# Kernel tuning notes

Hardware: AMD Instinct MI355X
Metric: run time of the kernel (lower is better)

Reference implementation:

```python
import jax, jax.numpy as jnp
import numpy as np

B, S, D = 4, 4096, 2048


def setup_inputs() -> dict:
    key = jax.random.key(0)
    ks = jax.random.split(key, 9)
    std = 1.0 / np.sqrt(D)
    inp = {
        "x": jax.random.normal(ks[0], (B, S, D), dtype=jnp.float32),
        "Wq": jax.random.normal(ks[1], (D, D), dtype=jnp.float32) * std,
        "bq": jnp.zeros((D,), dtype=jnp.float32),
        "Wk": jax.random.normal(ks[2], (D, D), dtype=jnp.float32) * std,
        "bk": jnp.zeros((D,), dtype=jnp.float32),
        "Wv": jax.random.normal(ks[3], (D, D), dtype=jnp.float32) * std,
        "bv": jnp.zeros((D,), dtype=jnp.float32),
        "Wo": jax.random.normal(ks[4], (D, D), dtype=jnp.float32) * std,
        "bo": jnp.zeros((D,), dtype=jnp.float32),
        "num_heads": 16,
        "num_groups": 4,
    }
    return inp


def reference(x, Wq, bq, Wk, bk, Wv, bv, Wo, bo, num_heads, num_groups):
    b, s, d = x.shape
    H = num_heads
    G = num_groups
    hd = d // H  # head_dim

    q = (x @ Wq + bq).reshape(b, s, H, hd)
    k = (x @ Wk + bk).reshape(b, s, H, hd)
    v = (x @ Wv + bv).reshape(b, s, H, hd)

    # GQA head permutation of queries: [B,S,G,H/G,Dh] -> transpose(2,3) -> [B,S,H,Dh]
    q = q.reshape(b, s, G, H // G, hd).transpose(0, 1, 3, 2, 4).reshape(b, s, H, hd)

    # NOTE: faithful to the source, scores are [B,S,H,H] (attention over heads
    # at each token, NOT over sequence positions), since q/k/v stay [B,S,H,Dh].
    scale = 1.0 / jnp.asarray(hd, x.dtype) ** 0.5
    scores = jnp.einsum('bshd,bstd->bsht', q, k) * scale  # [B,S,H,H]
    probs = jax.nn.softmax(scores, axis=-1)
    attn = jnp.einsum('bsht,bstd->bshd', probs, v)  # [B,S,H,Dh]

    out = attn.reshape(b, s, d) @ Wo + bo
    return out
```

## Files before the change

### kernel.cpp

```cpp
#include <hip/hip_runtime.h>
#include <stdint.h>

#define M_DIM 16384
#define D_DIM 2048
#define HEADS 16
#define HDIM 128

typedef __attribute__((ext_vector_type(8))) short bf16x8;
typedef __attribute__((ext_vector_type(4))) float f32x4;

__device__ __forceinline__ unsigned short f2bf(float f) {
  union { float f; uint32_t u; } c; c.f = f;
  uint32_t u = c.u;
  u += 0x7FFFu + ((u >> 16) & 1u);
  return (unsigned short)(u >> 16);
}
__device__ __forceinline__ float bf2f(unsigned short h) {
  union { float f; uint32_t u; } c; c.u = ((uint32_t)h) << 16;
  return c.f;
}

__device__ __forceinline__ void gload_lds16(const unsigned short* g, unsigned short* l) {
  __builtin_amdgcn_global_load_lds(
      (const __attribute__((address_space(1))) void*)g,
      (__attribute__((address_space(3))) void*)l,
      16, 0, 0);
}

__global__ __launch_bounds__(256) void cvt_x_kernel(const float4* __restrict__ in,
                                                    unsigned short* __restrict__ out,
                                                    int n4) {
  int i = blockIdx.x * blockDim.x + threadIdx.x;
  int stride = gridDim.x * blockDim.x;
  for (; i < n4; i += stride) {
    float4 v = in[i];
    ushort4 o;
    o.x = f2bf(v.x); o.y = f2bf(v.y); o.z = f2bf(v.z); o.w = f2bf(v.w);
    ((ushort4*)out)[i] = o;
  }
}

__global__ __launch_bounds__(256) void cvt_wt_kernel(const float* __restrict__ W0,
                                                     const float* __restrict__ W1,
                                                     const float* __restrict__ W2,
                                                     const float* __restrict__ W3,
                                                     unsigned short* __restrict__ Wt) {
  __shared__ float tile[32][33];
  const int z = blockIdx.z;
  const float* W = z == 0 ? W0 : (z == 1 ? W1 : (z == 2 ? W2 : W3));
  unsigned short* dst = Wt + (size_t)z * D_DIM * D_DIM;
  const int tx = threadIdx.x, ty = threadIdx.y;
  const int n0 = blockIdx.x * 32, k0 = blockIdx.y * 32;
  #pragma unroll
  for (int i = 0; i < 4; ++i)
    tile[ty + i * 8][tx] = W[(size_t)(k0 + ty + i * 8) * D_DIM + n0 + tx];
  __syncthreads();
  #pragma unroll
  for (int i = 0; i < 4; ++i)
    dst[(size_t)(n0 + ty + i * 8) * D_DIM + k0 + tx] = f2bf(tile[tx][ty + i * 8]);
}


#define SYNC_MID()                                          \
  do {                                                      \
    __builtin_amdgcn_sched_barrier(0);                      \
    __builtin_amdgcn_s_barrier();                           \
    asm volatile("s_waitcnt lgkmcnt(0)" ::: "memory");      \
    __builtin_amdgcn_sched_barrier(0);                      \
  } while (0)

#define SYNC_END()                                          \
  do {                                                      \
    __builtin_amdgcn_sched_barrier(0);                      \
    __builtin_amdgcn_s_barrier();                           \
    __builtin_amdgcn_sched_barrier(0);                      \
  } while (0)

#define READ_A(buf, mh, AF)                                               \
  do {                                                                    \
    const char* _ab = (const char*)&lds[buf][0][0];                       \
    _Pragma("unroll") for (int m = 0; m < 4; ++m) {                       \
      _Pragma("unroll") for (int kk = 0; kk < 2; ++kk) {                  \
        AF[m * 2 + kk] = *(const bf16x8*)(_ab +                           \
            (wm * 128 + (mh) * 64 + m * 16 + fr) * 128 +                  \
            (((kk * 4 + lk8) ^ swz) << 4));                               \
      }                                                                   \
    }                                                                     \
  } while (0)

#define READ_B(buf, nh, BF)                                               \
  do {                                                                    \
    const char* _bb = (const char*)&lds[buf][1][0];                       \
    _Pragma("unroll") for (int n = 0; n < 2; ++n) {                       \
      _Pragma("unroll") for (int kk = 0; kk < 2; ++kk) {                  \
        BF[n * 2 + kk] = *(const bf16x8*)(_bb +                           \
            (wn * 64 + (nh) * 32 + n * 16 + fr) * 128 +                   \
            (((kk * 4 + lk8) ^ swz) << 4));                               \
      }                                                                   \
    }                                                                     \
  } while (0)

#define MFMA_Q(mh, nh, AF, BF)                                            \
  do {                                                                    \
    _Pragma("unroll") for (int m = 0; m < 4; ++m) {                       \
      _Pragma("unroll") for (int n = 0; n < 2; ++n) {                     \
        _Pragma("unroll") for (int kk = 0; kk < 2; ++kk) {                \
          acc[(mh) * 4 + m][(nh) * 2 + n] =                               \
              __builtin_amdgcn_mfma_f32_16x16x32_bf16(                    \
                  AF[m * 2 + kk], BF[n * 2 + kk],                         \
                  acc[(mh) * 4 + m][(nh) * 2 + n], 0, 0, 0);              \
        }                                                                 \
      }                                                                   \
    }                                                                     \
  } while (0)

template<bool QKV>
__global__ __launch_bounds__(512, 2) void gemm256_kernel(
    const unsigned short* __restrict__ A,
    const unsigned short* __restrict__ Bt,
    const float* __restrict__ bias0,
    const float* __restrict__ bias1,
    const float* __restrict__ bias2,
    void* __restrict__ outp) {
  constexpr int K = 2048;
  constexpr int NT = 32;
  __shared__ __align__(16) unsigned short lds[2][2][16384];

  const int tid = threadIdx.x;
  const int wave = tid >> 6;
  const int lane = tid & 63;
  const int fr = lane & 15;
  const int lk8 = lane >> 4;
  const int wm = wave >> 2;
  const int wn = wave & 3;
  const int swz = fr & 7;

  const int nwg = gridDim.x;
  const int orig = blockIdx.x;
  const int wg = (orig & 7) * (nwg >> 3) + (orig >> 3);
  const int mi = wg & 63;
  const int ni = wg >> 6;

  const unsigned short* Ag = A + (size_t)(mi * 256) * K;
  const unsigned short* Bg = Bt + (size_t)(ni * 256) * K;
  const int k8s = (lane & 7) ^ (lane >> 3);

  auto stageA = [&](int tt, int half) {
    unsigned short* dst = &lds[tt & 1][0][0];
    #pragma unroll
    for (int j = 0; j < 2; ++j) {
      const int c = wave * 128 + j * 64 + lane;
      const int r = half * 128 + (c >> 3);
      gload_lds16(Ag + (size_t)r * K + tt * 64 + k8s * 8,
                  dst + (size_t)(half * 1024 + c) * 8);
    }
  };
  auto stageB = [&](int tt, int half) {
    unsigned short* dst = &lds[tt & 1][1][0];
    #pragma unroll
    for (int j = 0; j < 2; ++j) {
      const int c = wave * 128 + j * 64 + lane;
      const int r = half * 128 + (c >> 3);
      gload_lds16(Bg + (size_t)r * K + tt * 64 + k8s * 8,
                  dst + (size_t)(half * 1024 + c) * 8);
    }
  };

  f32x4 acc[8][4];
  #pragma unroll
  for (int m = 0; m < 8; ++m)
    #pragma unroll
    for (int n = 0; n < 4; ++n)
      acc[m][n] = (f32x4){0.f, 0.f, 0.f, 0.f};

  stageA(0, 0); stageA(0, 1); stageB(0, 0); stageB(0, 1);
  stageA(1, 0); stageA(1, 1);
  asm volatile("s_waitcnt vmcnt(4)" ::: "memory");
  __builtin_amdgcn_s_barrier();

  bf16x8 af0[8], af1[8], bf[4];
  #pragma unroll 1
  for (int t = 0; t < NT; t += 2) {
    READ_A(0, 0, af0); READ_B(0, 0, bf);
    stageB(t + 1, 0);
    SYNC_MID();
    __builtin_amdgcn_s_setprio(1); MFMA_Q(0, 0, af0, bf); __builtin_amdgcn_s_setprio(0);
    SYNC_END();
    READ_A(0, 1, af1);
    stageB(t + 1, 1);
    SYNC_MID();
    __builtin_amdgcn_s_setprio(1); MFMA_Q(1, 0, af1, bf); __builtin_amdgcn_s_setprio(0);
    SYNC_END();
    READ_B(0, 1, bf);
    if (t + 2 < NT) stageA(t + 2, 0);
    SYNC_MID();
    __builtin_amdgcn_s_setprio(1); MFMA_Q(1, 1, af1, bf); __builtin_amdgcn_s_setprio(0);
    SYNC_END();
    if (t + 2 < NT) stageA(t + 2, 1);
    SYNC_MID();
    __builtin_amdgcn_s_setprio(1); MFMA_Q(0, 1, af0, bf); __builtin_amdgcn_s_setprio(0);
    if (t + 2 < NT) { asm volatile("s_waitcnt vmcnt(4)" ::: "memory"); }
    else            { asm volatile("s_waitcnt vmcnt(0)" ::: "memory"); }
    SYNC_END();
    READ_A(1, 0, af0); READ_B(1, 0, bf);
    if (t + 2 < NT) stageB(t + 2, 0);
    SYNC_MID();
    __builtin_amdgcn_s_setprio(1); MFMA_Q(0, 0, af0, bf); __builtin_amdgcn_s_setprio(0);
    SYNC_END();
    READ_A(1, 1, af1);
    if (t + 2 < NT) stageB(t + 2, 1);
    SYNC_MID();
    __builtin_amdgcn_s_setprio(1); MFMA_Q(1, 0, af1, bf); __builtin_amdgcn_s_setprio(0);
    SYNC_END();
    READ_B(1, 1, bf);
    if (t + 3 < NT) stageA(t + 3, 0);
    SYNC_MID();
    __builtin_amdgcn_s_setprio(1); MFMA_Q(1, 1, af1, bf); __builtin_amdgcn_s_setprio(0);
    SYNC_END();
    if (t + 3 < NT) stageA(t + 3, 1);
    SYNC_MID();
    __builtin_amdgcn_s_setprio(1); MFMA_Q(0, 1, af0, bf); __builtin_amdgcn_s_setprio(0);
    if (t + 3 < NT) { asm volatile("s_waitcnt vmcnt(4)" ::: "memory"); }
    SYNC_END();
  }

  const int rb = mi * 256 + wm * 128 + (lane >> 4) * 4;
  const int cb = ni * 256 + wn * 64 + fr;
  if constexpr (QKV) {
    const int plane = (ni * 256) >> 11;
    const float* bias = plane == 0 ? bias0 : (plane == 1 ? bias1 : bias2);
    unsigned short* out = (unsigned short*)outp + (size_t)plane * M_DIM * D_DIM;
    #pragma unroll
    for (int n4 = 0; n4 < 4; ++n4) {
      const int col = (cb + n4 * 16) & (D_DIM - 1);
      const float bv = bias[col];
      #pragma unroll
      for (int m8 = 0; m8 < 8; ++m8)
        #pragma unroll
        for (int e = 0; e < 4; ++e)
          __builtin_nontemporal_store(f2bf(acc[m8][n4][e] + bv),
                                      &out[(size_t)(rb + m8 * 16 + e) * D_DIM + col]);
    }
  } else {
    float* out = (float*)outp;
    #pragma unroll
    for (int n4 = 0; n4 < 4; ++n4) {
      const int col = cb + n4 * 16;
      const float bv = bias0[col];
      #pragma unroll
      for (int m8 = 0; m8 < 8; ++m8)
        #pragma unroll
        for (int e = 0; e < 4; ++e)
          __builtin_nontemporal_store(acc[m8][n4][e] + bv,
                                      &out[(size_t)(rb + m8 * 16 + e) * D_DIM + col]);
    }
  }
}

__global__ __launch_bounds__(256) void attn_kernel(const unsigned short* __restrict__ qkv,
                                                   unsigned short* __restrict__ attnb) {
  __shared__ __align__(16) unsigned short kv_s[4][2][HEADS * HDIM];
  const int tid = threadIdx.x;
  const int wave = tid >> 6;
  const int lane = tid & 63;
  const int t = blockIdx.x * 4 + wave;
  const size_t MD = (size_t)M_DIM * D_DIM;

  const bf16x8* kg = (const bf16x8*)(qkv + MD + (size_t)t * D_DIM);
  const bf16x8* vg = (const bf16x8*)(qkv + 2 * MD + (size_t)t * D_DIM);
  bf16x8* ks = (bf16x8*)&kv_s[wave][0][0];
  bf16x8* vs = (bf16x8*)&kv_s[wave][1][0];
  #pragma unroll
  for (int i = 0; i < 4; ++i) {
    ks[i * 64 + lane] = kg[i * 64 + lane];
    vs[i * 64 + lane] = vg[i * 64 + lane];
  }

  const int ih = lane >> 2;
  const int qd = lane & 3;
  const int hsrc = (ih & 3) * 4 + (ih >> 2);
  const unsigned short* qg = qkv + (size_t)t * D_DIM + hsrc * HDIM + qd * 32;
  float qreg[32];
  #pragma unroll
  for (int c = 0; c < 4; ++c) {
    bf16x8 q8 = ((const bf16x8*)qg)[c];
    #pragma unroll
    for (int e = 0; e < 8; ++e) qreg[c * 8 + e] = bf2f((unsigned short)q8[e]);
  }

  __syncthreads();

  float s[16];
  #pragma unroll
  for (int j = 0; j < 16; ++j) {
    float acc = 0.f;
    const bf16x8* kp = (const bf16x8*)&kv_s[wave][0][j * HDIM + qd * 32];
    #pragma unroll
    for (int c = 0; c < 4; ++c) {
      bf16x8 k8 = kp[c];
      #pragma unroll
      for (int e = 0; e < 8; ++e) acc = fmaf(qreg[c * 8 + e], bf2f((unsigned short)k8[e]), acc);
    }
    acc += __shfl_xor(acc, 1);
    acc += __shfl_xor(acc, 2);
    s[j] = acc * 0.08838834764831845f;
  }

  float mx = s[0];
  #pragma unroll
  for (int j = 1; j < 16; ++j) mx = fmaxf(mx, s[j]);
  float sum = 0.f;
  #pragma unroll
  for (int j = 0; j < 16; ++j) { s[j] = __expf(s[j] - mx); sum += s[j]; }
  const float inv = 1.f / sum;

  float o[32];
  #pragma unroll
  for (int c = 0; c < 32; ++c) o[c] = 0.f;
  #pragma unroll
  for (int j = 0; j < 16; ++j) {
    const float p = s[j] * inv;
    const bf16x8* vp = (const bf16x8*)&kv_s[wave][1][j * HDIM + qd * 32];
    #pragma unroll
    for (int c = 0; c < 4; ++c) {
      bf16x8 v8 = vp[c];
      #pragma unroll
      for (int e = 0; e < 8; ++e) o[c * 8 + e] = fmaf(p, bf2f((unsigned short)v8[e]), o[c * 8 + e]);
    }
  }

  unsigned short* op = attnb + (size_t)t * D_DIM + ih * HDIM + qd * 32;
  #pragma unroll
  for (int c = 0; c < 4; ++c) {
    bf16x8 ov;
    #pragma unroll
    for (int e = 0; e < 8; ++e) ov[e] = (short)f2bf(o[c * 8 + e]);
    ((bf16x8*)op)[c] = ov;
  }
}

extern "C" void kernel_launch(void* const* d_in, const int* in_sizes, int n_in,
                              void* d_out, int out_size, void* d_ws, size_t ws_size,
                              hipStream_t stream) {
  const float* x  = (const float*)d_in[0];
  const float* Wq = (const float*)d_in[1];
  const float* bq = (const float*)d_in[2];
  const float* Wk = (const float*)d_in[3];
  const float* bk = (const float*)d_in[4];
  const float* Wv = (const float*)d_in[5];
  const float* bv = (const float*)d_in[6];
  const float* Wo = (const float*)d_in[7];
  const float* bo = (const float*)d_in[8];

  const size_t MD = (size_t)M_DIM * D_DIM;
  const size_t DD = (size_t)D_DIM * D_DIM;

  unsigned short* xb   = (unsigned short*)d_ws;
  unsigned short* Wt   = xb + MD;
  unsigned short* qkvb = Wt + 4 * DD;
  const size_t need_bytes = (MD + 4 * DD + 3 * MD) * sizeof(unsigned short);
  if (ws_size < need_bytes) return;

  cvt_x_kernel<<<2048, 256, 0, stream>>>((const float4*)x, xb, (int)(MD / 4));

  cvt_wt_kernel<<<dim3(64, 64, 4), dim3(32, 8), 0, stream>>>(Wq, Wk, Wv, Wo, Wt);

  gemm256_kernel<true><<<64 * 24, 512, 0, stream>>>(xb, Wt, bq, bk, bv, qkvb);

  attn_kernel<<<4096, 256, 0, stream>>>(qkvb, xb);

  gemm256_kernel<false><<<64 * 8, 512, 0, stream>>>(xb, Wt + 3 * DD, bo, nullptr, nullptr, d_out);
}
```

Baseline: 682.2 us.

## Reorder GEMM main loop to overlap LDS fragment reads with MFMA

Restructures the 8-phase GEMM main loop so LDS fragment reads for the next quadrant are issued inside the MFMA priority window of the current one. The first A fragment is prefetched before the loop, and the MFMA quadrant order is changed to (0,0),(1,0),(0,1),(1,1). Global staging is reordered ahead of the B reads, with vmcnt waits tightened to 2. The epilogue uses plain stores instead of nontemporal stores. This aims to hide LDS latency behind matrix math, but the tighter waits and the changed read/write ordering against barriers risk stalls or hazards.

```diff
diff --git a/kernel.cpp b/kernel.cpp
--- a/kernel.cpp
+++ b/kernel.cpp
@@ -176,51 +176,73 @@
   stageA(0, 0); stageA(0, 1); stageB(0, 0); stageB(0, 1);
   stageA(1, 0); stageA(1, 1);
   asm volatile("s_waitcnt vmcnt(4)" ::: "memory");
+  __builtin_amdgcn_sched_barrier(0);
   __builtin_amdgcn_s_barrier();
+  __builtin_amdgcn_sched_barrier(0);
 
   bf16x8 af0[8], af1[8], bf[4];
+  READ_A(0, 0, af0);
+
   #pragma unroll 1
   for (int t = 0; t < NT; t += 2) {
-    READ_A(0, 0, af0); READ_B(0, 0, bf);
     stageB(t + 1, 0);
-    SYNC_MID();
-    __builtin_amdgcn_s_setprio(1); MFMA_Q(0, 0, af0, bf); __builtin_amdgcn_s_setprio(0);
-    SYNC_END();
+    READ_B(0, 0, bf);
+    SYNC_MID();
+    __builtin_amdgcn_s_setprio(1);
+    MFMA_Q(0, 0, af0, bf);
     READ_A(0, 1, af1);
+    __builtin_amdgcn_s_setprio(0);
+    SYNC_END();
     stageB(t + 1, 1);
     SYNC_MID();
-    __builtin_amdgcn_s_setprio(1); MFMA_Q(1, 0, af1, bf); __builtin_amdgcn_s_setprio(0);
-    SYNC_END();
+    __builtin_amdgcn_s_setprio(1);
+    MFMA_Q(1, 0, af1, bf);
+    __builtin_amdgcn_s_setprio(0);
+    SYNC_END();
+    if (t + 2 < NT) stageA(t + 2, 0);
     READ_B(0, 1, bf);
-    if (t + 2 < NT) stageA(t + 2, 0);
-    SYNC_MID();
-    __builtin_amdgcn_s_setprio(1); MFMA_Q(1, 1, af1, bf); __builtin_amdgcn_s_setprio(0);
+    SYNC_MID();
+    __builtin_amdgcn_s_setprio(1);
+    MFMA_Q(0, 1, af0, bf);
+    __builtin_amdgcn_s_setprio(0);
+    if (t + 2 < NT) { asm volatile("s_waitcnt vmcnt(2)" ::: "memory"); }
+    else            { asm volatile("s_waitcnt vmcnt(0)" ::: "memory"); }
     SYNC_END();
     if (t + 2 < NT) stageA(t + 2, 1);
     SYNC_MID();
-    __builtin_amdgcn_s_setprio(1); MFMA_Q(0, 1, af0, bf); __builtin_amdgcn_s_setprio(0);
-    if (t + 2 < NT) { asm volatile("s_waitcnt vmcnt(4)" ::: "memory"); }
-    else            { asm volatile("s_waitcnt vmcnt(0)" ::: "memory"); }
-    SYNC_END();
-    READ_A(1, 0, af0); READ_B(1, 0, bf);
+    __builtin_amdgcn_s_setprio(1);
+    MFMA_Q(1, 1, af1, bf);
+    READ_A(1, 0, af0);
+    __builtin_amdgcn_s_setprio(0);
+    SYNC_END();
     if (t + 2 < NT) stageB(t + 2, 0);
-    SYNC_MID();
-    __builtin_amdgcn_s_setprio(1); MFMA_Q(0, 0, af0, bf); __builtin_amdgcn_s_setprio(0);
-    SYNC_END();
+    READ_B(1, 0, bf);
+    SYNC_MID();
+    __builtin_amdgcn_s_setprio(1);
+    MFMA_Q(0, 0, af0, bf);
     READ_A(1, 1, af1);
+    __builtin_amdgcn_s_setprio(0);
+    SYNC_END();
     if (t + 2 < NT) stageB(t + 2, 1);
     SYNC_MID();
-    __builtin_amdgcn_s_setprio(1); MFMA_Q(1, 0, af1, bf); __builtin_amdgcn_s_setprio(0);
-    SYNC_END();
+    __builtin_amdgcn_s_setprio(1);
+    MFMA_Q(1, 0, af1, bf);
+    __builtin_amdgcn_s_setprio(0);
+    SYNC_END();
+    if (t + 3 < NT) stageA(t + 3, 0);
     READ_B(1, 1, bf);
-    if (t + 3 < NT) stageA(t + 3, 0);
-    SYNC_MID();
-    __builtin_amdgcn_s_setprio(1); MFMA_Q(1, 1, af1, bf); __builtin_amdgcn_s_setprio(0);
+    SYNC_MID();
+    __builtin_amdgcn_s_setprio(1);
+    MFMA_Q(0, 1, af0, bf);
+    __builtin_amdgcn_s_setprio(0);
+    if (t + 2 < NT) { asm volatile("s_waitcnt vmcnt(2)" ::: "memory"); }
     SYNC_END();
     if (t + 3 < NT) stageA(t + 3, 1);
     SYNC_MID();
-    __builtin_amdgcn_s_setprio(1); MFMA_Q(0, 1, af0, bf); __builtin_amdgcn_s_setprio(0);
-    if (t + 3 < NT) { asm volatile("s_waitcnt vmcnt(4)" ::: "memory"); }
+    __builtin_amdgcn_s_setprio(1);
+    MFMA_Q(1, 1, af1, bf);
+    if (t + 2 < NT) READ_A(0, 0, af0);
+    __builtin_amdgcn_s_setprio(0);
     SYNC_END();
   }
 
@@ -238,8 +260,7 @@
       for (int m8 = 0; m8 < 8; ++m8)
         #pragma unroll
         for (int e = 0; e < 4; ++e)
-          __builtin_nontemporal_store(f2bf(acc[m8][n4][e] + bv),
-                                      &out[(size_t)(rb + m8 * 16 + e) * D_DIM + col]);
+          out[(size_t)(rb + m8 * 16 + e) * D_DIM + col] = f2bf(acc[m8][n4][e] + bv);
     }
   } else {
     float* out = (float*)outp;
@@ -251,8 +272,7 @@
       for (int m8 = 0; m8 < 8; ++m8)
         #pragma unroll
         for (int e = 0; e < 4; ++e)
-          __builtin_nontemporal_store(acc[m8][n4][e] + bv,
-                                      &out[(size_t)(rb + m8 * 16 + e) * D_DIM + col]);
+          out[(size_t)(rb + m8 * 16 + e) * D_DIM + col] = acc[m8][n4][e] + bv;
     }
   }
 }
```

After: 641.2 us. 6.0% less time.
